# Optimization experiments

Measured on AMD Instinct MI355X. Metric: run time of the kernel, lower is better.

The kernel has to match this reference:

```python
import jax, jax.numpy as jnp
import numpy as np

C = 256
C8 = C // 8

def setup_inputs() -> dict:
    key = jax.random.key(0)
    ks = jax.random.split(key, 7)
    B, H, W = 4, 64, 64
    x = jax.random.normal(ks[0], (B, C, H, W), dtype=jnp.float32)
    s = 1.0 / np.sqrt(C)
    Wq = jax.random.normal(ks[1], (C8, C), dtype=jnp.float32) * s
    bq = jnp.zeros((C8,), dtype=jnp.float32)
    Wk = jax.random.normal(ks[2], (C8, C), dtype=jnp.float32) * s
    bk = jnp.zeros((C8,), dtype=jnp.float32)
    Wv = jax.random.normal(ks[3], (C, C), dtype=jnp.float32) * s
    bv = jnp.zeros((C,), dtype=jnp.float32)
    return {"x": x, "Wq": Wq, "bq": bq, "Wk": Wk, "bk": bk, "Wv": Wv, "bv": bv}

def reference(x, Wq, bq, Wk, bk, Wv, bv):
    B, Cc, H, W = x.shape
    xf = x.reshape(B, Cc, H * W)                      # [B, C, N]
    # 1x1 convs == per-pixel linear projections
    q = jnp.einsum('dc,bcn->bdn', Wq, xf) + bq[None, :, None]   # [B, C/8, N]
    k = jnp.einsum('dc,bcn->bdn', Wk, xf) + bk[None, :, None]   # [B, C/8, N]
    v = jnp.einsum('dc,bcn->bdn', Wv, xf) + bv[None, :, None]   # [B, C,   N]
    scores = jnp.einsum('bdi,bdj->bij', q, k)         # [B, N, N] (no scaling, matching source)
    attn = jax.nn.softmax(scores, axis=-1)
    out = jnp.einsum('bcj,bij->bci', v, attn)         # [B, C, N]
    return out.reshape(B, Cc, H, W) + x
```

## Files before the change

### kernel.cpp

```cpp
#include <hip/hip_runtime.h>
#include <math.h>

#define CCH   256
#define NPIX  4096
#define BATCH 4

typedef __attribute__((ext_vector_type(8))) short s16x8;
typedef __attribute__((ext_vector_type(4))) float f32x4;

__device__ __forceinline__ unsigned short f2bf(float f) {
    unsigned int u = __float_as_uint(f);
    u += 0x7fff + ((u >> 16) & 1);
    return (unsigned short)(u >> 16);
}
__device__ __forceinline__ float bf2f(unsigned short h) {
    return __uint_as_float(((unsigned int)h) << 16);
}

__device__ __forceinline__ size_t qk_addr(int b, int n, int d) {
    return ((((size_t)b * 256 + (n >> 4)) * 64 + ((d >> 3) << 4) + (n & 15)) << 3) + (d & 7);
}
__device__ __forceinline__ size_t v_addr(int b, int j, int c) {
    return ((((((size_t)b * 64 + (j >> 6)) * 16 + (c >> 4)) * 2 + ((j >> 5) & 1)) * 64
            + (((j >> 3) & 3) << 4) + (c & 15)) << 3) + (j & 7);
}

__global__ __launch_bounds__(64) void wcast_kernel(
    const float* __restrict__ Wq, const float* __restrict__ bq,
    const float* __restrict__ Wk, const float* __restrict__ bk,
    const float* __restrict__ Wv, const float* __restrict__ bv,
    unsigned short* __restrict__ wfh, unsigned short* __restrict__ wfl,
    float* __restrict__ bias_ws)
{
    const int rt = blockIdx.x;
    const int lane = threadIdx.x, l15 = lane & 15, quad = lane >> 4;
    const float *Ws, *bs; int roff; float scale = 1.0f;
    if (rt < 2)      { Ws = Wq; bs = bq; roff = rt * 16;      scale = 1.44269504f; }
    else if (rt < 4) { Ws = Wk; bs = bk; roff = (rt - 2) * 16; }
    else             { Ws = Wv; bs = bv; roff = (rt - 4) * 16; }

    const float* wrow = Ws + (size_t)(roff + l15) * CCH + quad * 8;
    for (int kb = 0; kb < 8; ++kb) {
        s16x8 h, l;
        #pragma unroll
        for (int d = 0; d < 8; ++d) {
            float wv = wrow[kb * 32 + d] * scale;
            unsigned short hh = f2bf(wv);
            h[d] = (short)hh;
            l[d] = (short)f2bf(wv - bf2f(hh));
        }
        *(s16x8*)&wfh[(((size_t)rt * 8 + kb) * 64 + lane) * 8] = h;
        if (rt < 4) *(s16x8*)&wfl[(((size_t)rt * 8 + kb) * 64 + lane) * 8] = l;
    }
    if (lane < 16) bias_ws[rt * 16 + lane] = bs[roff + lane] * scale;
}

__global__ __launch_bounds__(256, 4) void proj_kernel(
    const float* __restrict__ x,
    const unsigned short* __restrict__ wfh, const unsigned short* __restrict__ wfl,
    const float* __restrict__ bias_ws,
    unsigned short* __restrict__ q_hi, unsigned short* __restrict__ q_lo,
    unsigned short* __restrict__ k_hi, unsigned short* __restrict__ k_lo,
    unsigned short* __restrict__ v_frag)
{
    const int t = threadIdx.x;
    const int rh = t >> 6, lane = t & 63, l15 = lane & 15, quad = lane >> 4;
    const int b = blockIdx.y;
    const int nt = blockIdx.x;

    const float* xb = x + (size_t)b * CCH * NPIX + nt * 16 + l15;
    s16x8 xh[8], xl[8];
    #pragma unroll
    for (int kb = 0; kb < 8; ++kb) {
        s16x8 vh, vl;
        #pragma unroll
        for (int d = 0; d < 8; ++d) {
            float xv = xb[(size_t)(kb * 32 + quad * 8 + d) * NPIX];
            unsigned short h = f2bf(xv);
            vh[d] = (short)h;
            vl[d] = (short)f2bf(xv - bf2f(h));
        }
        xh[kb] = vh; xl[kb] = vl;
    }

    const int n = nt * 16 + l15;
    #pragma unroll 1
    for (int tt = 0; tt < 5; ++tt) {
        const int rt = rh * 5 + tt;
        if (rt < 4) {
            f32x4 acc0 = {0.f, 0.f, 0.f, 0.f};
            f32x4 acc1 = {0.f, 0.f, 0.f, 0.f};
            #pragma unroll
            for (int kb = 0; kb < 8; ++kb) {
                s16x8 ah = *(const s16x8*)&wfh[(((size_t)rt * 8 + kb) * 64 + lane) * 8];
                s16x8 al = *(const s16x8*)&wfl[(((size_t)rt * 8 + kb) * 64 + lane) * 8];
                acc0 = __builtin_amdgcn_mfma_f32_16x16x32_bf16(ah, xh[kb], acc0, 0, 0, 0);
                acc1 = __builtin_amdgcn_mfma_f32_16x16x32_bf16(ah, xl[kb], acc1, 0, 0, 0);
                acc1 = __builtin_amdgcn_mfma_f32_16x16x32_bf16(al, xh[kb], acc1, 0, 0, 0);
            }
            #pragma unroll
            for (int rr = 0; rr < 4; ++rr) {
                const int rloc = quad * 4 + rr;
                const float val = acc0[rr] + acc1[rr] + bias_ws[rt * 16 + rloc];
                unsigned short h = f2bf(val);
                unsigned short l = f2bf(val - bf2f(h));
                if (rt < 2) {
                    const size_t a = qk_addr(b, n, rt * 16 + rloc);
                    q_hi[a] = h; q_lo[a] = l;
                } else {
                    const size_t a = qk_addr(b, n, (rt - 2) * 16 + rloc);
                    k_hi[a] = h; k_lo[a] = l;
                }
            }
        } else {
            f32x4 acc = {0.f, 0.f, 0.f, 0.f};
            #pragma unroll
            for (int kb = 0; kb < 8; ++kb) {
                s16x8 ah = *(const s16x8*)&wfh[(((size_t)rt * 8 + kb) * 64 + lane) * 8];
                acc = __builtin_amdgcn_mfma_f32_16x16x32_bf16(ah, xh[kb], acc, 0, 0, 0);
            }
            #pragma unroll
            for (int rr = 0; rr < 4; ++rr) {
                const int rloc = quad * 4 + rr;
                const float val = acc[rr] + bias_ws[rt * 16 + rloc];
                v_frag[v_addr(b, n, (rt - 4) * 16 + rloc)] = f2bf(val);
            }
        }
    }
}

#define BARRIER_LGKM() do { \
    asm volatile("s_waitcnt lgkmcnt(0)" ::: "memory"); \
    __builtin_amdgcn_s_barrier(); \
    asm volatile("" ::: "memory"); \
} while (0)

#define QK_STEP(KFH, KFL, BUFC) do { \
    f32x4 a0 = __builtin_amdgcn_mfma_f32_16x16x32_bf16((KFH), qfl0, (f32x4){0.f,0.f,0.f,0.f}, 0, 0, 0); \
    a0 = __builtin_amdgcn_mfma_f32_16x16x32_bf16((KFL), qfh0, a0, 0, 0, 0); \
    a0 = __builtin_amdgcn_mfma_f32_16x16x32_bf16((KFH), qfh0, a0, 0, 0, 0); \
    f32x4 a1 = __builtin_amdgcn_mfma_f32_16x16x32_bf16((KFH), qfl1, (f32x4){0.f,0.f,0.f,0.f}, 0, 0, 0); \
    a1 = __builtin_amdgcn_mfma_f32_16x16x32_bf16((KFL), qfh1, a1, 0, 0, 0); \
    a1 = __builtin_amdgcn_mfma_f32_16x16x32_bf16((KFH), qfh1, a1, 0, 0, 0); \
    unsigned int u0 = __float_as_uint(__builtin_exp2f(a0[0])) + 0x8000u; \
    unsigned int u1 = __float_as_uint(__builtin_exp2f(a0[1])) + 0x8000u; \
    unsigned int u2 = __float_as_uint(__builtin_exp2f(a0[2])) + 0x8000u; \
    unsigned int u3 = __float_as_uint(__builtin_exp2f(a0[3])) + 0x8000u; \
    uint2 pv0; \
    pv0.x = __builtin_amdgcn_perm(u1, u0, 0x07060302u); \
    pv0.y = __builtin_amdgcn_perm(u3, u2, 0x07060302u); \
    *(uint2*)&shm.p[ih][jh][BUFC][0 * 2 + pfrag_jj][(prow * 16 + l15) * 8 + pcol] = pv0; \
    u0 = __float_as_uint(__builtin_exp2f(a1[0])) + 0x8000u; \
    u1 = __float_as_uint(__builtin_exp2f(a1[1])) + 0x8000u; \
    u2 = __float_as_uint(__builtin_exp2f(a1[2])) + 0x8000u; \
    u3 = __float_as_uint(__builtin_exp2f(a1[3])) + 0x8000u; \
    uint2 pv1; \
    pv1.x = __builtin_amdgcn_perm(u1, u0, 0x07060302u); \
    pv1.y = __builtin_amdgcn_perm(u3, u2, 0x07060302u); \
    *(uint2*)&shm.p[ih][jh][BUFC][1 * 2 + pfrag_jj][(prow * 16 + l15) * 8 + pcol] = pv1; \
} while (0)

#define ATTN_BODY(T, BUFC, KU_H, KU_L, KL_H, KL_L, DO_QK) do { \
    const int jt = jh * 32 + (T); \
     \
    const s16x8 pf0 = *(const s16x8*)&shm.p[ih][jh][BUFC][0][lane * 8]; \
    const s16x8 pf1 = *(const s16x8*)&shm.p[ih][jh][BUFC][1][lane * 8]; \
    const s16x8 pf2 = *(const s16x8*)&shm.p[ih][jh][BUFC][2][lane * 8]; \
    const s16x8 pf3 = *(const s16x8*)&shm.p[ih][jh][BUFC][3][lane * 8]; \
     \
    const size_t vbase = (((size_t)jt * 16 + ch * 4) * 2) * 512; \
    const s16x8 v0 = *(const s16x8*)(vb + vbase); \
    const s16x8 v1 = *(const s16x8*)(vb + vbase + 512); \
    const s16x8 v2 = *(const s16x8*)(vb + vbase + 1024); \
    const s16x8 v3 = *(const s16x8*)(vb + vbase + 1536); \
    if (DO_QK) { QK_STEP(KU_H, KU_L, (BUFC) ^ 1); } \
     \
    { \
        const int tpp = ((T) + 2 < 32) ? (T) + 2 : 0; \
        const size_t koff = (size_t)((jh * 32 + tpp) * 4 + ch) * 512; \
        KL_H = *(const s16x8*)(khb + koff); \
        KL_L = *(const s16x8*)(klb + koff); \
    } \
     \
    if (ch == 0) { \
        lacc = __builtin_amdgcn_mfma_f32_16x16x32_bf16(ones, pf0, lacc, 0, 0, 0); \
        lacc = __builtin_amdgcn_mfma_f32_16x16x32_bf16(ones, pf1, lacc, 0, 0, 0); \
    } else if (ch == 1) { \
        lacc = __builtin_amdgcn_mfma_f32_16x16x32_bf16(ones, pf2, lacc, 0, 0, 0); \
        lacc = __builtin_amdgcn_mfma_f32_16x16x32_bf16(ones, pf3, lacc, 0, 0, 0); \
    } \
     \
    const s16x8 v4 = *(const s16x8*)(vb + vbase + 2048); \
    const s16x8 v5 = *(const s16x8*)(vb + vbase + 2560); \
    const s16x8 v6 = *(const s16x8*)(vb + vbase + 3072); \
    const s16x8 v7 = *(const s16x8*)(vb + vbase + 3584); \
    __builtin_amdgcn_s_setprio(1); \
    acc[0] = __builtin_amdgcn_mfma_f32_16x16x32_bf16(v0, pf0, acc[0], 0, 0, 0); \
    acc[0] = __builtin_amdgcn_mfma_f32_16x16x32_bf16(v1, pf1, acc[0], 0, 0, 0); \
    acc[1] = __builtin_amdgcn_mfma_f32_16x16x32_bf16(v0, pf2, acc[1], 0, 0, 0); \
    acc[1] = __builtin_amdgcn_mfma_f32_16x16x32_bf16(v1, pf3, acc[1], 0, 0, 0); \
    acc[2] = __builtin_amdgcn_mfma_f32_16x16x32_bf16(v2, pf0, acc[2], 0, 0, 0); \
    acc[2] = __builtin_amdgcn_mfma_f32_16x16x32_bf16(v3, pf1, acc[2], 0, 0, 0); \
    acc[3] = __builtin_amdgcn_mfma_f32_16x16x32_bf16(v2, pf2, acc[3], 0, 0, 0); \
    acc[3] = __builtin_amdgcn_mfma_f32_16x16x32_bf16(v3, pf3, acc[3], 0, 0, 0); \
    acc[4] = __builtin_amdgcn_mfma_f32_16x16x32_bf16(v4, pf0, acc[4], 0, 0, 0); \
    acc[4] = __builtin_amdgcn_mfma_f32_16x16x32_bf16(v5, pf1, acc[4], 0, 0, 0); \
    acc[5] = __builtin_amdgcn_mfma_f32_16x16x32_bf16(v4, pf2, acc[5], 0, 0, 0); \
    acc[5] = __builtin_amdgcn_mfma_f32_16x16x32_bf16(v5, pf3, acc[5], 0, 0, 0); \
    acc[6] = __builtin_amdgcn_mfma_f32_16x16x32_bf16(v6, pf0, acc[6], 0, 0, 0); \
    acc[6] = __builtin_amdgcn_mfma_f32_16x16x32_bf16(v7, pf1, acc[6], 0, 0, 0); \
    acc[7] = __builtin_amdgcn_mfma_f32_16x16x32_bf16(v6, pf2, acc[7], 0, 0, 0); \
    acc[7] = __builtin_amdgcn_mfma_f32_16x16x32_bf16(v7, pf3, acc[7], 0, 0, 0); \
    __builtin_amdgcn_s_setprio(0); \
    BARRIER_LGKM(); \
} while (0)

union AttnShMem {
    unsigned short p[2][2][2][4][512];
    f32x4 comb[2][2][4][2][64];
};

__global__ __launch_bounds__(1024, 4) void attn_kernel(
    const unsigned short* __restrict__ q_hi, const unsigned short* __restrict__ q_lo,
    const unsigned short* __restrict__ k_hi, const unsigned short* __restrict__ k_lo,
    const unsigned short* __restrict__ v_frag,
    const float* __restrict__ x, float* __restrict__ out)
{
    __shared__ AttnShMem shm;
    __shared__ float lds_l[2][2][2][16];

    const int t = threadIdx.x;
    const int w = t >> 6, lane = t & 63, l15 = lane & 15, quad = lane >> 4;
    const int ih = w >> 3, jh = (w >> 2) & 1, ch = w & 3;

    const int f = blockIdx.x;
    const int xcd = f & 7;
    const int b = xcd >> 1;
    const int ib = ((xcd & 1) << 5) + (f >> 3);

    s16x8 qfh0, qfl0, qfh1, qfl1;
    {
        const int ti0 = ib * 4 + ih * 2;
        const size_t qo0 = ((size_t)b * 256 + ti0 + 0) * 512 + (size_t)lane * 8;
        const size_t qo1 = ((size_t)b * 256 + ti0 + 1) * 512 + (size_t)lane * 8;
        qfh0 = *(const s16x8*)(q_hi + qo0);  qfl0 = *(const s16x8*)(q_lo + qo0);
        qfh1 = *(const s16x8*)(q_hi + qo1);  qfl1 = *(const s16x8*)(q_lo + qo1);
    }

    const s16x8 ones = { (short)0x3F80, (short)0x3F80, (short)0x3F80, (short)0x3F80,
                         (short)0x3F80, (short)0x3F80, (short)0x3F80, (short)0x3F80 };

    f32x4 acc[8];
    #pragma unroll
    for (int i = 0; i < 8; ++i) acc[i] = (f32x4){0.f, 0.f, 0.f, 0.f};
    f32x4 lacc = {0.f, 0.f, 0.f, 0.f};

    const unsigned short* khb = k_hi + (size_t)b * 131072 + (size_t)lane * 8;
    const unsigned short* klb = k_lo + (size_t)b * 131072 + (size_t)lane * 8;
    const unsigned short* vb  = v_frag + (size_t)b * 1048576 + (size_t)lane * 8;

    const int prow = ((ch & 1) << 1) + (quad >> 1);
    const int pcol = ((quad & 1) << 2);
    const int pfrag_jj = ch >> 1;

    s16x8 ka_h, ka_l, kb_h, kb_l;
    {
        const size_t k0 = (size_t)((jh * 32 + 0) * 4 + ch) * 512;
        ka_h = *(const s16x8*)(khb + k0);
        ka_l = *(const s16x8*)(klb + k0);
    }
    QK_STEP(ka_h, ka_l, 0);
    {
        const size_t k1 = (size_t)((jh * 32 + 1) * 4 + ch) * 512;
        ka_h = *(const s16x8*)(khb + k1);
        ka_l = *(const s16x8*)(klb + k1);
    }
    BARRIER_LGKM();

    #pragma unroll 1
    for (int t2 = 0; t2 < 16; ++t2) {
        ATTN_BODY(2 * t2,     0, ka_h, ka_l, kb_h, kb_l, 1);
        ATTN_BODY(2 * t2 + 1, 1, kb_h, kb_l, ka_h, ka_l, (t2 < 15));
    }

    if (ch < 2 && lane < 16) lds_l[ih][jh][ch][lane] = lacc[0];
    if (jh == 0) { shm.comb[ih][0][ch][0][lane] = acc[1]; shm.comb[ih][0][ch][1][lane] = acc[3]; }
    else         { shm.comb[ih][1][ch][0][lane] = acc[0]; shm.comb[ih][1][ch][1][lane] = acc[2]; }
    __syncthreads();
    const float linv = 1.f / (lds_l[ih][0][jh][l15] + lds_l[ih][1][jh][l15]);
    const int ibase = (ib * 4 + ih * 2 + jh) * 16 + l15;
    {
        f32x4 a0 = (jh == 0) ? acc[0] : acc[1];
        f32x4 a1 = (jh == 0) ? acc[2] : acc[3];
        a0 += shm.comb[ih][1 - jh][ch][0][lane];
        a1 += shm.comb[ih][1 - jh][ch][1][lane];
        #pragma unroll
        for (int rr = 0; rr < 4; ++rr) {
            const int c0 = ch * 64 + 0 * 16 + quad * 4 + rr;
            const int c1 = ch * 64 + 1 * 16 + quad * 4 + rr;
            const size_t i0 = ((size_t)b * CCH + c0) * NPIX + ibase;
            const size_t i1 = ((size_t)b * CCH + c1) * NPIX + ibase;
            out[i0] = a0[rr] * linv + x[i0];
            out[i1] = a1[rr] * linv + x[i1];
        }
    }
    __syncthreads();
    if (jh == 0) { shm.comb[ih][0][ch][0][lane] = acc[5]; shm.comb[ih][0][ch][1][lane] = acc[7]; }
    else         { shm.comb[ih][1][ch][0][lane] = acc[4]; shm.comb[ih][1][ch][1][lane] = acc[6]; }
    __syncthreads();
    {
        f32x4 a2 = (jh == 0) ? acc[4] : acc[5];
        f32x4 a3 = (jh == 0) ? acc[6] : acc[7];
        a2 += shm.comb[ih][1 - jh][ch][0][lane];
        a3 += shm.comb[ih][1 - jh][ch][1][lane];
        #pragma unroll
        for (int rr = 0; rr < 4; ++rr) {
            const int c2 = ch * 64 + 2 * 16 + quad * 4 + rr;
            const int c3 = ch * 64 + 3 * 16 + quad * 4 + rr;
            const size_t i2 = ((size_t)b * CCH + c2) * NPIX + ibase;
            const size_t i3 = ((size_t)b * CCH + c3) * NPIX + ibase;
            out[i2] = a2[rr] * linv + x[i2];
            out[i3] = a3[rr] * linv + x[i3];
        }
    }
}

extern "C" void kernel_launch(void* const* d_in, const int* in_sizes, int n_in,
                              void* d_out, int out_size, void* d_ws, size_t ws_size,
                              hipStream_t stream) {
    const float* x  = (const float*)d_in[0];
    const float* Wq = (const float*)d_in[1];
    const float* bq = (const float*)d_in[2];
    const float* Wk = (const float*)d_in[3];
    const float* bk = (const float*)d_in[4];
    const float* Wv = (const float*)d_in[5];
    const float* bv = (const float*)d_in[6];
    float* out = (float*)d_out;

    unsigned short* ws = (unsigned short*)d_ws;
    unsigned short* q_hi   = ws;
    unsigned short* q_lo   = ws + 524288;
    unsigned short* k_hi   = ws + 1048576;
    unsigned short* k_lo   = ws + 1572864;
    unsigned short* v_frag = ws + 2097152;
    unsigned short* wfh    = ws + 6291456;
    unsigned short* wfl    = ws + 6373376;
    float*          bias_ws = (float*)(ws + 6389760);

    wcast_kernel<<<20, 64, 0, stream>>>(Wq, bq, Wk, bk, Wv, bv, wfh, wfl, bias_ws);
    proj_kernel<<<dim3(256, BATCH), 256, 0, stream>>>(x, wfh, wfl, bias_ws,
                                                      q_hi, q_lo, k_hi, k_lo, v_frag);
    attn_kernel<<<256, 1024, 0, stream>>>(q_hi, q_lo, k_hi, k_lo, v_frag, x, out);
}
```

Measured before the change: 169.7 us.

## Fuse weight cast, projection and attention into one cooperative kernel

Merges the three launches into a single cooperative kernel that uses grid-wide syncs between the weight-cast, projection and attention phases, removing two kernel launch gaps. The projection is restructured so each wave streams x per k-block and computes one Q/K tile plus four V tiles, instead of caching all of x in registers and looping over five row tiles. Q/K stores are vectorised. The attention barrier moves to mid-body so the LDS wait overlaps the second half of the V loads. It falls back to the three-kernel path if the cooperative launch fails, and grid sync cost plus 1024-thread blocks in the projection phase may limit the gain.

```diff
diff --git a/kernel.cpp b/kernel.cpp
--- a/kernel.cpp
+++ b/kernel.cpp
@@ -1,11 +1,15 @@
 #include <hip/hip_runtime.h>
+#include <hip/hip_cooperative_groups.h>
 #include <math.h>
+
+namespace cg = cooperative_groups;
 
 #define CCH   256
 #define NPIX  4096
 #define BATCH 4
 
 typedef __attribute__((ext_vector_type(8))) short s16x8;
+typedef __attribute__((ext_vector_type(4))) short s16x4;
 typedef __attribute__((ext_vector_type(4))) float f32x4;
 
 __device__ __forceinline__ unsigned short f2bf(float f) {
@@ -25,37 +29,37 @@
             + (((j >> 3) & 3) << 4) + (c & 15)) << 3) + (j & 7);
 }
 
-__global__ __launch_bounds__(64) void wcast_kernel(
+
+__device__ __forceinline__ void wcast_unit(
+    const int rt, const int kb, const int lane, const bool do_bias,
     const float* __restrict__ Wq, const float* __restrict__ bq,
     const float* __restrict__ Wk, const float* __restrict__ bk,
     const float* __restrict__ Wv, const float* __restrict__ bv,
     unsigned short* __restrict__ wfh, unsigned short* __restrict__ wfl,
     float* __restrict__ bias_ws)
 {
-    const int rt = blockIdx.x;
-    const int lane = threadIdx.x, l15 = lane & 15, quad = lane >> 4;
+    const int l15 = lane & 15, quad = lane >> 4;
     const float *Ws, *bs; int roff; float scale = 1.0f;
     if (rt < 2)      { Ws = Wq; bs = bq; roff = rt * 16;      scale = 1.44269504f; }
     else if (rt < 4) { Ws = Wk; bs = bk; roff = (rt - 2) * 16; }
     else             { Ws = Wv; bs = bv; roff = (rt - 4) * 16; }
 
     const float* wrow = Ws + (size_t)(roff + l15) * CCH + quad * 8;
-    for (int kb = 0; kb < 8; ++kb) {
-        s16x8 h, l;
-        #pragma unroll
-        for (int d = 0; d < 8; ++d) {
-            float wv = wrow[kb * 32 + d] * scale;
-            unsigned short hh = f2bf(wv);
-            h[d] = (short)hh;
-            l[d] = (short)f2bf(wv - bf2f(hh));
-        }
-        *(s16x8*)&wfh[(((size_t)rt * 8 + kb) * 64 + lane) * 8] = h;
-        if (rt < 4) *(s16x8*)&wfl[(((size_t)rt * 8 + kb) * 64 + lane) * 8] = l;
-    }
-    if (lane < 16) bias_ws[rt * 16 + lane] = bs[roff + lane] * scale;
-}
-
-__global__ __launch_bounds__(256, 4) void proj_kernel(
+    s16x8 h, l;
+    #pragma unroll
+    for (int d = 0; d < 8; ++d) {
+        float wv = wrow[kb * 32 + d] * scale;
+        unsigned short hh = f2bf(wv);
+        h[d] = (short)hh;
+        l[d] = (short)f2bf(wv - bf2f(hh));
+    }
+    *(s16x8*)&wfh[(((size_t)rt * 8 + kb) * 64 + lane) * 8] = h;
+    if (rt < 4) *(s16x8*)&wfl[(((size_t)rt * 8 + kb) * 64 + lane) * 8] = l;
+    if (do_bias && lane < 16) bias_ws[rt * 16 + lane] = bs[roff + lane] * scale;
+}
+
+__device__ __forceinline__ void proj_unit(
+    const int pb, const int nt, const int rh, const int lane,
     const float* __restrict__ x,
     const unsigned short* __restrict__ wfh, const unsigned short* __restrict__ wfl,
     const float* __restrict__ bias_ws,
@@ -63,71 +67,77 @@
     unsigned short* __restrict__ k_hi, unsigned short* __restrict__ k_lo,
     unsigned short* __restrict__ v_frag)
 {
-    const int t = threadIdx.x;
-    const int rh = t >> 6, lane = t & 63, l15 = lane & 15, quad = lane >> 4;
-    const int b = blockIdx.y;
-    const int nt = blockIdx.x;
-
-    const float* xb = x + (size_t)b * CCH * NPIX + nt * 16 + l15;
-    s16x8 xh[8], xl[8];
+    const int l15 = lane & 15, quad = lane >> 4;
+    const float* xb = x + (size_t)pb * CCH * NPIX + nt * 16 + l15;
+
+    f32x4 aq0 = {0.f, 0.f, 0.f, 0.f};
+    f32x4 aq1 = {0.f, 0.f, 0.f, 0.f};
+    f32x4 av[4];
     #pragma unroll
+    for (int i = 0; i < 4; ++i) av[i] = (f32x4){0.f, 0.f, 0.f, 0.f};
+
+    #pragma unroll 2
     for (int kb = 0; kb < 8; ++kb) {
-        s16x8 vh, vl;
+        s16x8 xh, xl;
         #pragma unroll
         for (int d = 0; d < 8; ++d) {
             float xv = xb[(size_t)(kb * 32 + quad * 8 + d) * NPIX];
             unsigned short h = f2bf(xv);
-            vh[d] = (short)h;
-            vl[d] = (short)f2bf(xv - bf2f(h));
-        }
-        xh[kb] = vh; xl[kb] = vl;
+            xh[d] = (short)h;
+            xl[d] = (short)f2bf(xv - bf2f(h));
+        }
+        {
+            const s16x8 ah = *(const s16x8*)&wfh[(((size_t)rh * 8 + kb) * 64 + lane) * 8];
+            const s16x8 al = *(const s16x8*)&wfl[(((size_t)rh * 8 + kb) * 64 + lane) * 8];
+            aq0 = __builtin_amdgcn_mfma_f32_16x16x32_bf16(ah, xh, aq0, 0, 0, 0);
+            aq1 = __builtin_amdgcn_mfma_f32_16x16x32_bf16(ah, xl, aq1, 0, 0, 0);
+            aq1 = __builtin_amdgcn_mfma_f32_16x16x32_bf16(al, xh, aq1, 0, 0, 0);
+        }
+        #pragma unroll
+        for (int i = 0; i < 4; ++i) {
+            const int rt = 4 + rh * 4 + i;
+            const s16x8 ah = *(const s16x8*)&wfh[(((size_t)rt * 8 + kb) * 64 + lane) * 8];
+            av[i] = __builtin_amdgcn_mfma_f32_16x16x32_bf16(ah, xh, av[i], 0, 0, 0);
+        }
     }
 
     const int n = nt * 16 + l15;
-    #pragma unroll 1
-    for (int tt = 0; tt < 5; ++tt) {
-        const int rt = rh * 5 + tt;
-        if (rt < 4) {
-            f32x4 acc0 = {0.f, 0.f, 0.f, 0.f};
-            f32x4 acc1 = {0.f, 0.f, 0.f, 0.f};
-            #pragma unroll
-            for (int kb = 0; kb < 8; ++kb) {
-                s16x8 ah = *(const s16x8*)&wfh[(((size_t)rt * 8 + kb) * 64 + lane) * 8];
-                s16x8 al = *(const s16x8*)&wfl[(((size_t)rt * 8 + kb) * 64 + lane) * 8];
-                acc0 = __builtin_amdgcn_mfma_f32_16x16x32_bf16(ah, xh[kb], acc0, 0, 0, 0);
-                acc1 = __builtin_amdgcn_mfma_f32_16x16x32_bf16(ah, xl[kb], acc1, 0, 0, 0);
-                acc1 = __builtin_amdgcn_mfma_f32_16x16x32_bf16(al, xh[kb], acc1, 0, 0, 0);
-            }
-            #pragma unroll
-            for (int rr = 0; rr < 4; ++rr) {
-                const int rloc = quad * 4 + rr;
-                const float val = acc0[rr] + acc1[rr] + bias_ws[rt * 16 + rloc];
-                unsigned short h = f2bf(val);
-                unsigned short l = f2bf(val - bf2f(h));
-                if (rt < 2) {
-                    const size_t a = qk_addr(b, n, rt * 16 + rloc);
-                    q_hi[a] = h; q_lo[a] = l;
-                } else {
-                    const size_t a = qk_addr(b, n, (rt - 2) * 16 + rloc);
-                    k_hi[a] = h; k_lo[a] = l;
-                }
-            }
+    {
+        s16x4 h4, l4;
+        #pragma unroll
+        for (int rr = 0; rr < 4; ++rr) {
+            const int rloc = quad * 4 + rr;
+            const float val = aq0[rr] + aq1[rr] + bias_ws[rh * 16 + rloc];
+            const unsigned short h = f2bf(val);
+            h4[rr] = (short)h;
+            l4[rr] = (short)f2bf(val - bf2f(h));
+        }
+        if (rh < 2) {
+            const size_t a = qk_addr(pb, n, rh * 16 + quad * 4);
+            *(s16x4*)&q_hi[a] = h4;
+            *(s16x4*)&q_lo[a] = l4;
         } else {
-            f32x4 acc = {0.f, 0.f, 0.f, 0.f};
-            #pragma unroll
-            for (int kb = 0; kb < 8; ++kb) {
-                s16x8 ah = *(const s16x8*)&wfh[(((size_t)rt * 8 + kb) * 64 + lane) * 8];
-                acc = __builtin_amdgcn_mfma_f32_16x16x32_bf16(ah, xh[kb], acc, 0, 0, 0);
-            }
-            #pragma unroll
-            for (int rr = 0; rr < 4; ++rr) {
-                const int rloc = quad * 4 + rr;
-                const float val = acc[rr] + bias_ws[rt * 16 + rloc];
-                v_frag[v_addr(b, n, (rt - 4) * 16 + rloc)] = f2bf(val);
-            }
-        }
-    }
-}
+            const size_t a = qk_addr(pb, n, (rh - 2) * 16 + quad * 4);
+            *(s16x4*)&k_hi[a] = h4;
+            *(s16x4*)&k_lo[a] = l4;
+        }
+    }
+    #pragma unroll
+    for (int i = 0; i < 4; ++i) {
+        const int vt = rh * 4 + i;
+        #pragma unroll
+        for (int rr = 0; rr < 4; ++rr) {
+            const int rloc = quad * 4 + rr;
+            const float val = av[i][rr] + bias_ws[(4 + vt) * 16 + rloc];
+            v_frag[v_addr(pb, n, vt * 16 + rloc)] = f2bf(val);
+        }
+    }
+}
+
+union AttnShMem {
+    unsigned short p[2][2][2][4][512];
+    f32x4 comb[2][2][4][2][64];
+};
 
 #define BARRIER_LGKM() do { \
     asm volatile("s_waitcnt lgkmcnt(0)" ::: "memory"); \
@@ -146,42 +156,38 @@
     unsigned int u1 = __float_as_uint(__builtin_exp2f(a0[1])) + 0x8000u; \
     unsigned int u2 = __float_as_uint(__builtin_exp2f(a0[2])) + 0x8000u; \
     unsigned int u3 = __float_as_uint(__builtin_exp2f(a0[3])) + 0x8000u; \
-    uint2 pv0; \
-    pv0.x = __builtin_amdgcn_perm(u1, u0, 0x07060302u); \
-    pv0.y = __builtin_amdgcn_perm(u3, u2, 0x07060302u); \
-    *(uint2*)&shm.p[ih][jh][BUFC][0 * 2 + pfrag_jj][(prow * 16 + l15) * 8 + pcol] = pv0; \
+    uint2 pv; \
+    pv.x = __builtin_amdgcn_perm(u1, u0, 0x07060302u); \
+    pv.y = __builtin_amdgcn_perm(u3, u2, 0x07060302u); \
+    *(uint2*)&shm.p[ih][jh][BUFC][0 * 2 + pfrag_jj][(prow * 16 + l15) * 8 + pcol] = pv; \
     u0 = __float_as_uint(__builtin_exp2f(a1[0])) + 0x8000u; \
     u1 = __float_as_uint(__builtin_exp2f(a1[1])) + 0x8000u; \
     u2 = __float_as_uint(__builtin_exp2f(a1[2])) + 0x8000u; \
     u3 = __float_as_uint(__builtin_exp2f(a1[3])) + 0x8000u; \
-    uint2 pv1; \
-    pv1.x = __builtin_amdgcn_perm(u1, u0, 0x07060302u); \
-    pv1.y = __builtin_amdgcn_perm(u3, u2, 0x07060302u); \
-    *(uint2*)&shm.p[ih][jh][BUFC][1 * 2 + pfrag_jj][(prow * 16 + l15) * 8 + pcol] = pv1; \
+    uint2 pw; \
+    pw.x = __builtin_amdgcn_perm(u1, u0, 0x07060302u); \
+    pw.y = __builtin_amdgcn_perm(u3, u2, 0x07060302u); \
+    *(uint2*)&shm.p[ih][jh][BUFC][1 * 2 + pfrag_jj][(prow * 16 + l15) * 8 + pcol] = pw; \
 } while (0)
 
 #define ATTN_BODY(T, BUFC, KU_H, KU_L, KL_H, KL_L, DO_QK) do { \
     const int jt = jh * 32 + (T); \
-     \
     const s16x8 pf0 = *(const s16x8*)&shm.p[ih][jh][BUFC][0][lane * 8]; \
     const s16x8 pf1 = *(const s16x8*)&shm.p[ih][jh][BUFC][1][lane * 8]; \
     const s16x8 pf2 = *(const s16x8*)&shm.p[ih][jh][BUFC][2][lane * 8]; \
     const s16x8 pf3 = *(const s16x8*)&shm.p[ih][jh][BUFC][3][lane * 8]; \
-     \
     const size_t vbase = (((size_t)jt * 16 + ch * 4) * 2) * 512; \
     const s16x8 v0 = *(const s16x8*)(vb + vbase); \
     const s16x8 v1 = *(const s16x8*)(vb + vbase + 512); \
     const s16x8 v2 = *(const s16x8*)(vb + vbase + 1024); \
     const s16x8 v3 = *(const s16x8*)(vb + vbase + 1536); \
     if (DO_QK) { QK_STEP(KU_H, KU_L, (BUFC) ^ 1); } \
-     \
     { \
         const int tpp = ((T) + 2 < 32) ? (T) + 2 : 0; \
         const size_t koff = (size_t)((jh * 32 + tpp) * 4 + ch) * 512; \
         KL_H = *(const s16x8*)(khb + koff); \
         KL_L = *(const s16x8*)(klb + koff); \
     } \
-     \
     if (ch == 0) { \
         lacc = __builtin_amdgcn_mfma_f32_16x16x32_bf16(ones, pf0, lacc, 0, 0, 0); \
         lacc = __builtin_amdgcn_mfma_f32_16x16x32_bf16(ones, pf1, lacc, 0, 0, 0); \
@@ -189,7 +195,7 @@
         lacc = __builtin_amdgcn_mfma_f32_16x16x32_bf16(ones, pf2, lacc, 0, 0, 0); \
         lacc = __builtin_amdgcn_mfma_f32_16x16x32_bf16(ones, pf3, lacc, 0, 0, 0); \
     } \
-     \
+    BARRIER_LGKM(); \
     const s16x8 v4 = *(const s16x8*)(vb + vbase + 2048); \
     const s16x8 v5 = *(const s16x8*)(vb + vbase + 2560); \
     const s16x8 v6 = *(const s16x8*)(vb + vbase + 3072); \
@@ -212,28 +218,18 @@
     acc[7] = __builtin_amdgcn_mfma_f32_16x16x32_bf16(v6, pf2, acc[7], 0, 0, 0); \
     acc[7] = __builtin_amdgcn_mfma_f32_16x16x32_bf16(v7, pf3, acc[7], 0, 0, 0); \
     __builtin_amdgcn_s_setprio(0); \
-    BARRIER_LGKM(); \
 } while (0)
 
-union AttnShMem {
-    unsigned short p[2][2][2][4][512];
-    f32x4 comb[2][2][4][2][64];
-};
-
-__global__ __launch_bounds__(1024, 4) void attn_kernel(
+__device__ __forceinline__ void attn_impl(
+    const int f, const int t, AttnShMem& shm, float (&lds_l)[2][2][2][16],
     const unsigned short* __restrict__ q_hi, const unsigned short* __restrict__ q_lo,
     const unsigned short* __restrict__ k_hi, const unsigned short* __restrict__ k_lo,
     const unsigned short* __restrict__ v_frag,
     const float* __restrict__ x, float* __restrict__ out)
 {
-    __shared__ AttnShMem shm;
-    __shared__ float lds_l[2][2][2][16];
-
-    const int t = threadIdx.x;
     const int w = t >> 6, lane = t & 63, l15 = lane & 15, quad = lane >> 4;
     const int ih = w >> 3, jh = (w >> 2) & 1, ch = w & 3;
 
-    const int f = blockIdx.x;
     const int xcd = f & 7;
     const int b = xcd >> 1;
     const int ib = ((xcd & 1) << 5) + (f >> 3);
@@ -323,6 +319,84 @@
             out[i3] = a3[rr] * linv + x[i3];
         }
     }
+}
+
+__global__ __launch_bounds__(64) void wcast_kernel(
+    const float* __restrict__ Wq, const float* __restrict__ bq,
+    const float* __restrict__ Wk, const float* __restrict__ bk,
+    const float* __restrict__ Wv, const float* __restrict__ bv,
+    unsigned short* __restrict__ wfh, unsigned short* __restrict__ wfl,
+    float* __restrict__ bias_ws)
+{
+    const int rt = blockIdx.x, lane = threadIdx.x;
+    for (int kb = 0; kb < 8; ++kb)
+        wcast_unit(rt, kb, lane, kb == 0, Wq, bq, Wk, bk, Wv, bv, wfh, wfl, bias_ws);
+}
+
+__global__ __launch_bounds__(256, 4) void proj_kernel(
+    const float* __restrict__ x,
+    const unsigned short* __restrict__ wfh, const unsigned short* __restrict__ wfl,
+    const float* __restrict__ bias_ws,
+    unsigned short* __restrict__ q_hi, unsigned short* __restrict__ q_lo,
+    unsigned short* __restrict__ k_hi, unsigned short* __restrict__ k_lo,
+    unsigned short* __restrict__ v_frag)
+{
+    proj_unit(blockIdx.y, blockIdx.x, threadIdx.x >> 6, threadIdx.x & 63,
+              x, wfh, wfl, bias_ws, q_hi, q_lo, k_hi, k_lo, v_frag);
+}
+
+__global__ __launch_bounds__(1024, 4) void attn_kernel(
+    const unsigned short* __restrict__ q_hi, const unsigned short* __restrict__ q_lo,
+    const unsigned short* __restrict__ k_hi, const unsigned short* __restrict__ k_lo,
+    const unsigned short* __restrict__ v_frag,
+    const float* __restrict__ x, float* __restrict__ out)
+{
+    __shared__ AttnShMem shm;
+    __shared__ float lds_l[2][2][2][16];
+    attn_impl(blockIdx.x, threadIdx.x, shm, lds_l, q_hi, q_lo, k_hi, k_lo, v_frag, x, out);
+}
+
+__global__ __launch_bounds__(1024, 4) void fused_kernel(
+    const float* __restrict__ x,
+    const float* __restrict__ Wq, const float* __restrict__ bq,
+    const float* __restrict__ Wk, const float* __restrict__ bk,
+    const float* __restrict__ Wv, const float* __restrict__ bv,
+    unsigned short* __restrict__ wfh, unsigned short* __restrict__ wfl,
+    float* __restrict__ bias_ws,
+    unsigned short* __restrict__ q_hi, unsigned short* __restrict__ q_lo,
+    unsigned short* __restrict__ k_hi, unsigned short* __restrict__ k_lo,
+    unsigned short* __restrict__ v_frag,
+    float* __restrict__ out)
+{
+    __shared__ AttnShMem shm;
+    __shared__ float lds_l[2][2][2][16];
+
+    cg::grid_group grid = cg::this_grid();
+
+    const int t = threadIdx.x;
+    const int w = t >> 6, lane = t & 63;
+    const int f = blockIdx.x;
+
+    {
+        const int gw = f * 16 + w;
+        if (gw < 160)
+            wcast_unit(gw >> 3, gw & 7, lane, (gw & 7) == 0,
+                       Wq, bq, Wk, bk, Wv, bv, wfh, wfl, bias_ws);
+    }
+    __threadfence();
+    grid.sync();
+    __threadfence();
+
+    {
+        const int o = f * 4 + (w >> 2);
+        proj_unit(o >> 8, o & 255, w & 3, lane,
+                  x, wfh, wfl, bias_ws, q_hi, q_lo, k_hi, k_lo, v_frag);
+    }
+    __threadfence();
+    grid.sync();
+    __threadfence();
+
+    attn_impl(f, t, shm, lds_l, q_hi, q_lo, k_hi, k_lo, v_frag, x, out);
 }
 
 extern "C" void kernel_launch(void* const* d_in, const int* in_sizes, int n_in,
@@ -347,8 +421,20 @@
     unsigned short* wfl    = ws + 6373376;
     float*          bias_ws = (float*)(ws + 6389760);
 
-    wcast_kernel<<<20, 64, 0, stream>>>(Wq, bq, Wk, bk, Wv, bv, wfh, wfl, bias_ws);
-    proj_kernel<<<dim3(256, BATCH), 256, 0, stream>>>(x, wfh, wfl, bias_ws,
-                                                      q_hi, q_lo, k_hi, k_lo, v_frag);
-    attn_kernel<<<256, 1024, 0, stream>>>(q_hi, q_lo, k_hi, k_lo, v_frag, x, out);
-}
+    void* kargs[] = {
+        (void*)&x,
+        (void*)&Wq, (void*)&bq, (void*)&Wk, (void*)&bk, (void*)&Wv, (void*)&bv,
+        (void*)&wfh, (void*)&wfl, (void*)&bias_ws,
+        (void*)&q_hi, (void*)&q_lo, (void*)&k_hi, (void*)&k_lo, (void*)&v_frag,
+        (void*)&out
+    };
+    hipError_t e = hipLaunchCooperativeKernel((const void*)fused_kernel,
+                                              dim3(256), dim3(1024), kargs, 0, stream);
+    if (e != hipSuccess) {
+        (void)hipGetLastError();
+        wcast_kernel<<<20, 64, 0, stream>>>(Wq, bq, Wk, bk, Wv, bv, wfh, wfl, bias_ws);
+        proj_kernel<<<dim3(256, BATCH), 256, 0, stream>>>(x, wfh, wfl, bias_ws,
+                                                          q_hi, q_lo, k_hi, k_lo, v_frag);
+        attn_kernel<<<256, 1024, 0, stream>>>(q_hi, q_lo, k_hi, k_lo, v_frag, x, out);
+    }
+}
```

Result: slower. 546.1 us (+221.8%).
